# Kernel optimization log

Measured on AMD Instinct MI355X. Metric: run time of the kernel, lower is better.

Reference implementation:

```python
import jax, jax.numpy as jnp
import numpy as np

N_NODES = 50000
N_EDGES = 600000
D_FT = 128   # prompt_dim == node feature dim
D_E = 32     # edge feature dim


def setup_inputs() -> dict:
    key = jax.random.key(0)
    k1, k2, k3, k4, k5 = jax.random.split(key, 5)
    graph_embedding = jax.random.normal(k1, (N_NODES, D_FT), dtype=jnp.float32)
    e_feat = jax.random.normal(k2, (N_EDGES, D_E), dtype=jnp.float32)
    weight = jax.random.normal(k3, (1, D_FT), dtype=jnp.float32)  # learned prompt
    src_idx = jax.random.randint(k4, (N_EDGES,), 0, N_NODES)
    dst_idx = jax.random.randint(k5, (N_EDGES,), 0, N_NODES)
    return {"graph_embedding": graph_embedding, "e_feat": e_feat,
            "weight": weight, "src_idx": src_idx, "dst_idx": dst_idx}


def reference(graph_embedding, e_feat, weight, src_idx, dst_idx):
    # message m = concat(src_ft * p, e); dst_ft = segment_sum(m over dst).
    # concat commutes with segment-sum, so reduce the two halves separately
    # and concatenate at node level (avoids materializing [E, D_FT+D_E]).
    src_ft = graph_embedding[src_idx] * weight            # [E, D_FT]
    agg_ft = jax.ops.segment_sum(src_ft, dst_idx, num_segments=N_NODES)
    agg_e = jax.ops.segment_sum(e_feat, dst_idx, num_segments=N_NODES)
    return jnp.concatenate([agg_ft, agg_e], axis=1)      # [N, D_FT+D_E]
```

## Files before the change

kernel.cpp:

```cpp
#include <hip/hip_runtime.h>


#define D_FT 128
#define D_E 32
#define D_OUT (D_FT + D_E)
#define CAP 32

typedef float f32x4 __attribute__((ext_vector_type(4)));
typedef int   i32x2 __attribute__((ext_vector_type(2)));

__global__ void place_bucket_kernel(const int* __restrict__ src_idx,
                                    const int* __restrict__ dst_idx,
                                    int* __restrict__ cursor,
                                    i32x2* __restrict__ bucket,
                                    int* __restrict__ ovf,
                                    int* __restrict__ ovf_cnt, int E) {
    int i = blockIdx.x * blockDim.x + threadIdx.x;
    if (i >= E) return;
    int d = dst_idx[i];
    int slot = atomicAdd(&cursor[d], 1);
    if (slot < CAP) {
        i32x2 pr; pr.x = src_idx[i]; pr.y = i;
        bucket[(size_t)d * CAP + slot] = pr;
    } else {
        int p = atomicAdd(ovf_cnt, 1);
        ovf[p] = i;
    }
}

__global__ void gather_bucket_kernel(const float* __restrict__ emb,
                                     const float* __restrict__ e_feat,
                                     const float* __restrict__ w,
                                     const int* __restrict__ cursor,
                                     const i32x2* __restrict__ bucket,
                                     const int* __restrict__ src_idx,
                                     const int* __restrict__ dst_idx,
                                     const int* __restrict__ ovf,
                                     const int* __restrict__ ovf_cnt,
                                     float* __restrict__ out, int N) {
    int g = (blockIdx.x * blockDim.x + threadIdx.x) >> 6;
    if (g >= N) return;
    const int lane = threadIdx.x & 63;
    const int half = lane >> 5;
    const int q    = lane & 31;
    const int qg   = q >> 3;
    const int ql   = q & 7;

    i32x2 pr = bucket[(size_t)g * CAP + (lane & 31)];
    int cnt_raw = cursor[g];
    int cnt = cnt_raw > CAP ? CAP : cnt_raw;

    float4 accft = make_float4(0.f, 0.f, 0.f, 0.f);
    float4 acce  = make_float4(0.f, 0.f, 0.f, 0.f);

    int i = 0;
    if (cnt >= 8) {
        int b  = (half << 2);
        int s0 = __shfl(pr.x, b + 0, 64);
        int s1 = __shfl(pr.x, b + 1, 64);
        int s2 = __shfl(pr.x, b + 2, 64);
        int s3 = __shfl(pr.x, b + 3, 64);
        int ee = __shfl(pr.y, b + qg, 64);
        float4 v0 = *reinterpret_cast<const float4*>(emb + (size_t)s0 * D_FT + q * 4);
        float4 v1 = *reinterpret_cast<const float4*>(emb + (size_t)s1 * D_FT + q * 4);
        float4 v2 = *reinterpret_cast<const float4*>(emb + (size_t)s2 * D_FT + q * 4);
        float4 v3 = *reinterpret_cast<const float4*>(emb + (size_t)s3 * D_FT + q * 4);
        f32x4 a = __builtin_nontemporal_load(
            reinterpret_cast<const f32x4*>(e_feat + (size_t)ee * D_E + ql * 4));

        for (i = 8; i + 8 <= cnt; i += 8) {
            int b2 = i + (half << 2);
            int t0 = __shfl(pr.x, b2 + 0, 64);
            int t1 = __shfl(pr.x, b2 + 1, 64);
            int t2 = __shfl(pr.x, b2 + 2, 64);
            int t3 = __shfl(pr.x, b2 + 3, 64);
            int e2 = __shfl(pr.y, b2 + qg, 64);
            float4 u0 = *reinterpret_cast<const float4*>(emb + (size_t)t0 * D_FT + q * 4);
            float4 u1 = *reinterpret_cast<const float4*>(emb + (size_t)t1 * D_FT + q * 4);
            float4 u2 = *reinterpret_cast<const float4*>(emb + (size_t)t2 * D_FT + q * 4);
            float4 u3 = *reinterpret_cast<const float4*>(emb + (size_t)t3 * D_FT + q * 4);
            f32x4 a2 = __builtin_nontemporal_load(
                reinterpret_cast<const f32x4*>(e_feat + (size_t)e2 * D_E + ql * 4));
            accft.x += (v0.x + v1.x) + (v2.x + v3.x);
            accft.y += (v0.y + v1.y) + (v2.y + v3.y);
            accft.z += (v0.z + v1.z) + (v2.z + v3.z);
            accft.w += (v0.w + v1.w) + (v2.w + v3.w);
            acce.x += a.x; acce.y += a.y; acce.z += a.z; acce.w += a.w;
            v0 = u0; v1 = u1; v2 = u2; v3 = u3; a = a2;
        }
        accft.x += (v0.x + v1.x) + (v2.x + v3.x);
        accft.y += (v0.y + v1.y) + (v2.y + v3.y);
        accft.z += (v0.z + v1.z) + (v2.z + v3.z);
        accft.w += (v0.w + v1.w) + (v2.w + v3.w);
        acce.x += a.x; acce.y += a.y; acce.z += a.z; acce.w += a.w;
    }
    if (i < cnt) {
        const int c1 = cnt - 1;
        int b  = i + (half << 2);
        int t0 = b + 0, t1 = b + 1, t2 = b + 2, t3 = b + 3, te = b + qg;
        int s0 = __shfl(pr.x, t0 < c1 ? t0 : c1, 64);
        int s1 = __shfl(pr.x, t1 < c1 ? t1 : c1, 64);
        int s2 = __shfl(pr.x, t2 < c1 ? t2 : c1, 64);
        int s3 = __shfl(pr.x, t3 < c1 ? t3 : c1, 64);
        int ee = __shfl(pr.y, te < c1 ? te : c1, 64);
        float4 v0 = *reinterpret_cast<const float4*>(emb + (size_t)s0 * D_FT + q * 4);
        float4 v1 = *reinterpret_cast<const float4*>(emb + (size_t)s1 * D_FT + q * 4);
        float4 v2 = *reinterpret_cast<const float4*>(emb + (size_t)s2 * D_FT + q * 4);
        float4 v3 = *reinterpret_cast<const float4*>(emb + (size_t)s3 * D_FT + q * 4);
        f32x4 a = __builtin_nontemporal_load(
            reinterpret_cast<const f32x4*>(e_feat + (size_t)ee * D_E + ql * 4));
        float m0 = (t0 < cnt) ? 1.f : 0.f;
        float m1 = (t1 < cnt) ? 1.f : 0.f;
        float m2 = (t2 < cnt) ? 1.f : 0.f;
        float m3 = (t3 < cnt) ? 1.f : 0.f;
        float me = (te < cnt) ? 1.f : 0.f;
        accft.x = fmaf(v0.x, m0, accft.x); accft.y = fmaf(v0.y, m0, accft.y);
        accft.z = fmaf(v0.z, m0, accft.z); accft.w = fmaf(v0.w, m0, accft.w);
        accft.x = fmaf(v1.x, m1, accft.x); accft.y = fmaf(v1.y, m1, accft.y);
        accft.z = fmaf(v1.z, m1, accft.z); accft.w = fmaf(v1.w, m1, accft.w);
        accft.x = fmaf(v2.x, m2, accft.x); accft.y = fmaf(v2.y, m2, accft.y);
        accft.z = fmaf(v2.z, m2, accft.z); accft.w = fmaf(v2.w, m2, accft.w);
        accft.x = fmaf(v3.x, m3, accft.x); accft.y = fmaf(v3.y, m3, accft.y);
        accft.z = fmaf(v3.z, m3, accft.z); accft.w = fmaf(v3.w, m3, accft.w);
        acce.x = fmaf(a.x, me, acce.x); acce.y = fmaf(a.y, me, acce.y);
        acce.z = fmaf(a.z, me, acce.z); acce.w = fmaf(a.w, me, acce.w);
    }

    if (cnt_raw > CAP) {
        int n = *ovf_cnt;
        for (int k = 0; k < n; ++k) {
            int eid = ovf[k];
            if (dst_idx[eid] == g && half == 0) {
                int s = src_idx[eid];
                float4 v = *reinterpret_cast<const float4*>(emb + (size_t)s * D_FT + q * 4);
                accft.x += v.x; accft.y += v.y; accft.z += v.z; accft.w += v.w;
                if (q < 8) {
                    f32x4 a = *reinterpret_cast<const f32x4*>(e_feat + (size_t)eid * D_E + q * 4);
                    acce.x += a.x; acce.y += a.y; acce.z += a.z; acce.w += a.w;
                }
            }
        }
    }

    accft.x += __shfl_xor(accft.x, 32, 64);
    accft.y += __shfl_xor(accft.y, 32, 64);
    accft.z += __shfl_xor(accft.z, 32, 64);
    accft.w += __shfl_xor(accft.w, 32, 64);
    acce.x += __shfl_xor(acce.x, 8, 64);
    acce.y += __shfl_xor(acce.y, 8, 64);
    acce.z += __shfl_xor(acce.z, 8, 64);
    acce.w += __shfl_xor(acce.w, 8, 64);
    acce.x += __shfl_xor(acce.x, 16, 64);
    acce.y += __shfl_xor(acce.y, 16, 64);
    acce.z += __shfl_xor(acce.z, 16, 64);
    acce.w += __shfl_xor(acce.w, 16, 64);
    acce.x += __shfl_xor(acce.x, 32, 64);
    acce.y += __shfl_xor(acce.y, 32, 64);
    acce.z += __shfl_xor(acce.z, 32, 64);
    acce.w += __shfl_xor(acce.w, 32, 64);

    if (half == 0) {
        float4 wv = *reinterpret_cast<const float4*>(w + q * 4);
        float* o = out + (size_t)g * D_OUT;
        f32x4 r; r.x = accft.x * wv.x; r.y = accft.y * wv.y;
                 r.z = accft.z * wv.z; r.w = accft.w * wv.w;
        __builtin_nontemporal_store(r, reinterpret_cast<f32x4*>(o + q * 4));
        if (q < 8) {
            f32x4 re; re.x = acce.x; re.y = acce.y; re.z = acce.z; re.w = acce.w;
            __builtin_nontemporal_store(re, reinterpret_cast<f32x4*>(o + D_FT + q * 4));
        }
    }
}

__global__ void scatter_ft_kernel(const float* __restrict__ emb, const float* __restrict__ w,
                                  const int* __restrict__ src_idx, const int* __restrict__ dst_idx,
                                  float* __restrict__ out, int n_items) {
    int idx = blockIdx.x * blockDim.x + threadIdx.x;
    if (idx >= n_items) return;
    int e = idx >> 5, q = idx & 31;
    int s = src_idx[e], d = dst_idx[e];
    const float4 v  = *reinterpret_cast<const float4*>(emb + (size_t)s * D_FT + q * 4);
    const float4 wv = *reinterpret_cast<const float4*>(w + q * 4);
    float* o = out + (size_t)d * D_OUT + q * 4;
    atomicAdd(o + 0, v.x * wv.x); atomicAdd(o + 1, v.y * wv.y);
    atomicAdd(o + 2, v.z * wv.z); atomicAdd(o + 3, v.w * wv.w);
}
__global__ void scatter_e_kernel(const float* __restrict__ e_feat, const int* __restrict__ dst_idx,
                                 float* __restrict__ out, int n_items) {
    int idx = blockIdx.x * blockDim.x + threadIdx.x;
    if (idx >= n_items) return;
    int e = idx >> 3, q = idx & 7;
    int d = dst_idx[e];
    const float4 v = *reinterpret_cast<const float4*>(e_feat + (size_t)e * D_E + q * 4);
    float* o = out + (size_t)d * D_OUT + D_FT + q * 4;
    atomicAdd(o + 0, v.x); atomicAdd(o + 1, v.y);
    atomicAdd(o + 2, v.z); atomicAdd(o + 3, v.w);
}

extern "C" void kernel_launch(void* const* d_in, const int* in_sizes, int n_in,
                              void* d_out, int out_size, void* d_ws, size_t ws_size,
                              hipStream_t stream) {
    const float* emb    = (const float*)d_in[0];
    const float* e_feat = (const float*)d_in[1];
    const float* w      = (const float*)d_in[2];
    const int*   src    = (const int*)d_in[3];
    const int*   dst    = (const int*)d_in[4];
    float* out = (float*)d_out;

    const int E = in_sizes[3];
    const int N = out_size / D_OUT;

    size_t ints_head = (size_t)N + 2;
    size_t need = ints_head * 4 + (size_t)N * CAP * 8 + (size_t)E * 4;

    if (ws_size >= need) {
        int*   cursor  = (int*)d_ws;
        int*   ovf_cnt = cursor + N;
        i32x2* bucket  = (i32x2*)(cursor + ints_head);
        int*   ovf     = (int*)(bucket + (size_t)N * CAP);

        hipMemsetAsync(cursor, 0, ints_head * sizeof(int), stream);
        place_bucket_kernel<<<(E + 255) / 256, 256, 0, stream>>>(
            src, dst, cursor, bucket, ovf, ovf_cnt, E);
        gather_bucket_kernel<<<((size_t)N * 64 + 255) / 256, 256, 0, stream>>>(
            emb, e_feat, w, cursor, bucket, src, dst, ovf, ovf_cnt, out, N);
    } else {
        hipMemsetAsync(d_out, 0, (size_t)out_size * sizeof(float), stream);
        int items_ft = E * 32, items_e = E * 8;
        scatter_ft_kernel<<<(items_ft + 255) / 256, 256, 0, stream>>>(emb, w, src, dst, out, items_ft);
        scatter_e_kernel<<<(items_e + 255) / 256, 256, 0, stream>>>(e_feat, dst, out, items_e);
    }
}
```

Measured before the change: 99.96 us.

## Assign one node per half-wavefront instead of one per full wavefront in gather

The gather kernel now maps each destination node to 32 lanes instead of 64, so a wavefront processes two nodes. Each group walks its bucket four edges at a time, with no software-pipelined prefetch, and the cross-half reduction of the feature accumulator is dropped. This halves the thread count and removes idle lanes at the store stage. The trade-off is less memory-level parallelism per node and more serial loop iterations, since the unrolled prefetch loop is gone. With about 12 edges per node on average, divergence between the two nodes sharing a wavefront could also matter.

New measurement: 100.5 us. About the same (+0.5%).

```diff
diff --git a/kernel.cpp b/kernel.cpp
--- a/kernel.cpp
+++ b/kernel.cpp
@@ -38,15 +38,13 @@
                                      const int* __restrict__ ovf,
                                      const int* __restrict__ ovf_cnt,
                                      float* __restrict__ out, int N) {
-    int g = (blockIdx.x * blockDim.x + threadIdx.x) >> 6;
+    int g = (blockIdx.x * blockDim.x + threadIdx.x) >> 5;
     if (g >= N) return;
-    const int lane = threadIdx.x & 63;
-    const int half = lane >> 5;
-    const int q    = lane & 31;
-    const int qg   = q >> 3;
-    const int ql   = q & 7;
+    const int q  = threadIdx.x & 31;
+    const int qg = q >> 3;
+    const int ql = q & 7;
 
-    i32x2 pr = bucket[(size_t)g * CAP + (lane & 31)];
+    i32x2 pr = bucket[(size_t)g * CAP + q];
     int cnt_raw = cursor[g];
     int cnt = cnt_raw > CAP ? CAP : cnt_raw;
 
@@ -54,40 +52,18 @@
     float4 acce  = make_float4(0.f, 0.f, 0.f, 0.f);
 
     int i = 0;
-    if (cnt >= 8) {
-        int b  = (half << 2);
-        int s0 = __shfl(pr.x, b + 0, 64);
-        int s1 = __shfl(pr.x, b + 1, 64);
-        int s2 = __shfl(pr.x, b + 2, 64);
-        int s3 = __shfl(pr.x, b + 3, 64);
-        int ee = __shfl(pr.y, b + qg, 64);
+    for (; i + 4 <= cnt; i += 4) {
+        int s0 = __shfl(pr.x, i + 0, 32);
+        int s1 = __shfl(pr.x, i + 1, 32);
+        int s2 = __shfl(pr.x, i + 2, 32);
+        int s3 = __shfl(pr.x, i + 3, 32);
+        int ee = __shfl(pr.y, i + qg, 32);
         float4 v0 = *reinterpret_cast<const float4*>(emb + (size_t)s0 * D_FT + q * 4);
         float4 v1 = *reinterpret_cast<const float4*>(emb + (size_t)s1 * D_FT + q * 4);
         float4 v2 = *reinterpret_cast<const float4*>(emb + (size_t)s2 * D_FT + q * 4);
         float4 v3 = *reinterpret_cast<const float4*>(emb + (size_t)s3 * D_FT + q * 4);
         f32x4 a = __builtin_nontemporal_load(
             reinterpret_cast<const f32x4*>(e_feat + (size_t)ee * D_E + ql * 4));
-
-        for (i = 8; i + 8 <= cnt; i += 8) {
-            int b2 = i + (half << 2);
-            int t0 = __shfl(pr.x, b2 + 0, 64);
-            int t1 = __shfl(pr.x, b2 + 1, 64);
-            int t2 = __shfl(pr.x, b2 + 2, 64);
-            int t3 = __shfl(pr.x, b2 + 3, 64);
-            int e2 = __shfl(pr.y, b2 + qg, 64);
-            float4 u0 = *reinterpret_cast<const float4*>(emb + (size_t)t0 * D_FT + q * 4);
-            float4 u1 = *reinterpret_cast<const float4*>(emb + (size_t)t1 * D_FT + q * 4);
-            float4 u2 = *reinterpret_cast<const float4*>(emb + (size_t)t2 * D_FT + q * 4);
-            float4 u3 = *reinterpret_cast<const float4*>(emb + (size_t)t3 * D_FT + q * 4);
-            f32x4 a2 = __builtin_nontemporal_load(
-                reinterpret_cast<const f32x4*>(e_feat + (size_t)e2 * D_E + ql * 4));
-            accft.x += (v0.x + v1.x) + (v2.x + v3.x);
-            accft.y += (v0.y + v1.y) + (v2.y + v3.y);
-            accft.z += (v0.z + v1.z) + (v2.z + v3.z);
-            accft.w += (v0.w + v1.w) + (v2.w + v3.w);
-            acce.x += a.x; acce.y += a.y; acce.z += a.z; acce.w += a.w;
-            v0 = u0; v1 = u1; v2 = u2; v3 = u3; a = a2;
-        }
         accft.x += (v0.x + v1.x) + (v2.x + v3.x);
         accft.y += (v0.y + v1.y) + (v2.y + v3.y);
         accft.z += (v0.z + v1.z) + (v2.z + v3.z);
@@ -96,13 +72,12 @@
     }
     if (i < cnt) {
         const int c1 = cnt - 1;
-        int b  = i + (half << 2);
-        int t0 = b + 0, t1 = b + 1, t2 = b + 2, t3 = b + 3, te = b + qg;
-        int s0 = __shfl(pr.x, t0 < c1 ? t0 : c1, 64);
-        int s1 = __shfl(pr.x, t1 < c1 ? t1 : c1, 64);
-        int s2 = __shfl(pr.x, t2 < c1 ? t2 : c1, 64);
-        int s3 = __shfl(pr.x, t3 < c1 ? t3 : c1, 64);
-        int ee = __shfl(pr.y, te < c1 ? te : c1, 64);
+        int t0 = i + 0, t1 = i + 1, t2 = i + 2, t3 = i + 3, te = i + qg;
+        int s0 = __shfl(pr.x, t0 < c1 ? t0 : c1, 32);
+        int s1 = __shfl(pr.x, t1 < c1 ? t1 : c1, 32);
+        int s2 = __shfl(pr.x, t2 < c1 ? t2 : c1, 32);
+        int s3 = __shfl(pr.x, t3 < c1 ? t3 : c1, 32);
+        int ee = __shfl(pr.y, te < c1 ? te : c1, 32);
         float4 v0 = *reinterpret_cast<const float4*>(emb + (size_t)s0 * D_FT + q * 4);
         float4 v1 = *reinterpret_cast<const float4*>(emb + (size_t)s1 * D_FT + q * 4);
         float4 v2 = *reinterpret_cast<const float4*>(emb + (size_t)s2 * D_FT + q * 4);
@@ -130,7 +105,7 @@
         int n = *ovf_cnt;
         for (int k = 0; k < n; ++k) {
             int eid = ovf[k];
-            if (dst_idx[eid] == g && half == 0) {
+            if (dst_idx[eid] == g) {
                 int s = src_idx[eid];
                 float4 v = *reinterpret_cast<const float4*>(emb + (size_t)s * D_FT + q * 4);
                 accft.x += v.x; accft.y += v.y; accft.z += v.z; accft.w += v.w;
@@ -142,33 +117,23 @@
         }
     }
 
-    accft.x += __shfl_xor(accft.x, 32, 64);
-    accft.y += __shfl_xor(accft.y, 32, 64);
-    accft.z += __shfl_xor(accft.z, 32, 64);
-    accft.w += __shfl_xor(accft.w, 32, 64);
-    acce.x += __shfl_xor(acce.x, 8, 64);
-    acce.y += __shfl_xor(acce.y, 8, 64);
-    acce.z += __shfl_xor(acce.z, 8, 64);
-    acce.w += __shfl_xor(acce.w, 8, 64);
-    acce.x += __shfl_xor(acce.x, 16, 64);
-    acce.y += __shfl_xor(acce.y, 16, 64);
-    acce.z += __shfl_xor(acce.z, 16, 64);
-    acce.w += __shfl_xor(acce.w, 16, 64);
-    acce.x += __shfl_xor(acce.x, 32, 64);
-    acce.y += __shfl_xor(acce.y, 32, 64);
-    acce.z += __shfl_xor(acce.z, 32, 64);
-    acce.w += __shfl_xor(acce.w, 32, 64);
+    acce.x += __shfl_xor(acce.x, 8, 32);
+    acce.y += __shfl_xor(acce.y, 8, 32);
+    acce.z += __shfl_xor(acce.z, 8, 32);
+    acce.w += __shfl_xor(acce.w, 8, 32);
+    acce.x += __shfl_xor(acce.x, 16, 32);
+    acce.y += __shfl_xor(acce.y, 16, 32);
+    acce.z += __shfl_xor(acce.z, 16, 32);
+    acce.w += __shfl_xor(acce.w, 16, 32);
 
-    if (half == 0) {
-        float4 wv = *reinterpret_cast<const float4*>(w + q * 4);
-        float* o = out + (size_t)g * D_OUT;
-        f32x4 r; r.x = accft.x * wv.x; r.y = accft.y * wv.y;
-                 r.z = accft.z * wv.z; r.w = accft.w * wv.w;
-        __builtin_nontemporal_store(r, reinterpret_cast<f32x4*>(o + q * 4));
-        if (q < 8) {
-            f32x4 re; re.x = acce.x; re.y = acce.y; re.z = acce.z; re.w = acce.w;
-            __builtin_nontemporal_store(re, reinterpret_cast<f32x4*>(o + D_FT + q * 4));
-        }
+    float4 wv = *reinterpret_cast<const float4*>(w + q * 4);
+    float* o = out + (size_t)g * D_OUT;
+    f32x4 r; r.x = accft.x * wv.x; r.y = accft.y * wv.y;
+             r.z = accft.z * wv.z; r.w = accft.w * wv.w;
+    __builtin_nontemporal_store(r, reinterpret_cast<f32x4*>(o + q * 4));
+    if (q < 8) {
+        f32x4 re; re.x = acce.x; re.y = acce.y; re.z = acce.z; re.w = acce.w;
+        __builtin_nontemporal_store(re, reinterpret_cast<f32x4*>(o + D_FT + q * 4));
     }
 }
 
@@ -222,7 +187,7 @@
         hipMemsetAsync(cursor, 0, ints_head * sizeof(int), stream);
         place_bucket_kernel<<<(E + 255) / 256, 256, 0, stream>>>(
             src, dst, cursor, bucket, ovf, ovf_cnt, E);
-        gather_bucket_kernel<<<((size_t)N * 64 + 255) / 256, 256, 0, stream>>>(
+        gather_bucket_kernel<<<((size_t)N * 32 + 255) / 256, 256, 0, stream>>>(
             emb, e_feat, w, cursor, bucket, src, dst, ovf, ovf_cnt, out, N);
     } else {
         hipMemsetAsync(d_out, 0, (size_t)out_size * sizeof(float), stream);
```
